# Kernel tuning notes

Hardware: AMD Instinct MI355X
Metric: run time of the kernel (lower is better)

Reference implementation:

```python
import jax, jax.numpy as jnp
import numpy as np

NUM_FEATURES = 20480
NUM_ACC = 128
BATCH = 4096
SPARSITY_P = 0.0015  # ~30 active features per position, like real NNUE


def setup_inputs() -> dict:
    key = jax.random.key(0)
    kw, kb, k1, k2, k3, k4 = jax.random.split(key, 6)
    # sparse binary one-hot-per-piece feature vectors
    white = (jax.random.uniform(kw, (BATCH, NUM_FEATURES)) < SPARSITY_P).astype(jnp.float32)
    black = (jax.random.uniform(kb, (BATCH, NUM_FEATURES)) < SPARSITY_P).astype(jnp.float32)
    psqt_w = jax.random.normal(k1, (2, NUM_FEATURES), dtype=jnp.float32) * 0.02
    acc_w = jax.random.normal(k2, (NUM_ACC, NUM_FEATURES), dtype=jnp.float32) * 0.02
    acc_b = jax.random.normal(k3, (NUM_ACC,), dtype=jnp.float32) * 0.02
    out_w = jax.random.normal(k4, (2, NUM_ACC), dtype=jnp.float32) * 0.1
    return {"white": white, "black": black, "psqt_w": psqt_w,
            "acc_w": acc_w, "acc_b": acc_b, "out_w": out_w}


def _side(x, psqt_w, acc_w, acc_b, out_w):
    # psqt: [B,2]; accumulator: [B,128]; CReLU then Linear(128->2, no bias)
    psqt = x @ psqt_w.T                              # [B, 2]
    acc = jnp.clip(x @ acc_w.T + acc_b, 0.0, 1.0)    # [B, 128]
    pos = acc @ out_w.T                              # [B, 2]
    return psqt, pos


def reference(white, black, psqt_w, acc_w, acc_b, out_w):
    psqt_w_, pos_w = _side(white, psqt_w, acc_w, acc_b, out_w)
    psqt_b, pos_b = _side(black, psqt_w, acc_w, acc_b, out_w)
    return (psqt_w_ - psqt_b) + (pos_w - pos_b)      # [B, 2]
```

## Files before the change

### kernel.cpp

```cpp
#include <hip/hip_runtime.h>

#define NF    20480
#define NACC  128
#define BATCH 4096
#define MAXI  96

typedef unsigned int uvec4 __attribute__((ext_vector_type(4)));
typedef unsigned int uvec2 __attribute__((ext_vector_type(2)));
typedef float        fvec4 __attribute__((ext_vector_type(4)));

__device__ __forceinline__ float bflo(unsigned int w) {
    union { unsigned int u; float f; } v; v.u = w << 16; return v.f;
}
__device__ __forceinline__ float bfhi(unsigned int w) {
    union { unsigned int u; float f; } v; v.u = w & 0xFFFF0000u; return v.f;
}
__device__ __forceinline__ unsigned short f2bf(float f) {
    union { float f; unsigned int i; } v; v.f = f;
    unsigned int x = v.i;
    return (unsigned short)((x + 0x7FFFu + ((x >> 16) & 1u)) >> 16);
}

__global__ __launch_bounds__(256) void transpose_accw(const float* __restrict__ acc_w,
                                                      unsigned short* __restrict__ accT) {
    __shared__ float tile[NACC][33];
    const int t  = threadIdx.x;
    const int f0 = blockIdx.x * 32;
    const int fl = t & 31;
    const int cr = t >> 5;
    #pragma unroll
    for (int i = 0; i < 16; ++i) {
        int cc = i * 8 + cr;
        tile[cc][fl] = acc_w[(size_t)cc * NF + f0 + fl];
    }
    __syncthreads();
    const int c  = t & 127;
    const int fr = t >> 7;
    #pragma unroll
    for (int i = 0; i < 16; ++i) {
        int ff = i * 2 + fr;
        accT[(size_t)(f0 + ff) * NACC + c] = f2bf(tile[c][ff]);
    }
}

#define BALLOT_COMPACT(d, fidx)                                           \
    {                                                                     \
        unsigned long long m = __ballot((d) != 0u);                       \
        if (m) {                                                          \
            int pre  = __popcll(m & ((1ull << lane) - 1ull));             \
            int src  = (int)(__ffsll((unsigned long long)(m)) - 1);       \
            int base = 0;                                                 \
            if (lane == src) base = atomicAdd(cnt, __popcll(m));          \
            base = __shfl(base, src, 64);                                 \
            int slot = base + pre;                                        \
            if ((d) && slot < MAXI) idx[slot] = (fidx);                   \
        }                                                                 \
    }

#define PROC16(c0, c1, c2, c3, fb)                                        \
    BALLOT_COMPACT(c0.x, (fb) + 0)   BALLOT_COMPACT(c0.y, (fb) + 1)       \
    BALLOT_COMPACT(c0.z, (fb) + 2)   BALLOT_COMPACT(c0.w, (fb) + 3)       \
    BALLOT_COMPACT(c1.x, (fb) + 512) BALLOT_COMPACT(c1.y, (fb) + 513)     \
    BALLOT_COMPACT(c1.z, (fb) + 514) BALLOT_COMPACT(c1.w, (fb) + 515)     \
    BALLOT_COMPACT(c2.x, (fb) + 1024) BALLOT_COMPACT(c2.y, (fb) + 1025)   \
    BALLOT_COMPACT(c2.z, (fb) + 1026) BALLOT_COMPACT(c2.w, (fb) + 1027)   \
    BALLOT_COMPACT(c3.x, (fb) + 1536) BALLOT_COMPACT(c3.y, (fb) + 1537)   \
    BALLOT_COMPACT(c3.z, (fb) + 1538) BALLOT_COMPACT(c3.w, (fb) + 1539)

__global__ __launch_bounds__(256) void nnue_main(
    const float* __restrict__ white,
    const float* __restrict__ black,
    const float* __restrict__ psqt_w,
    const unsigned short* __restrict__ accT,
    const float* __restrict__ acc_b,
    const float* __restrict__ out_w,
    float* __restrict__ out)
{
    __shared__ int   s_cnt[2];
    __shared__ int   s_idx[2][MAXI];
    __shared__ fvec4 s_part[2][4][32];
    __shared__ float s_red[8];

    const int t    = threadIdx.x;
    const int b    = blockIdx.x;
    const int side = t >> 7;
    const int lt   = t & 127;
    const int lane = t & 63;

    const float bias = acc_b[lt];
    const float ow0  = out_w[lt];
    const float ow1  = out_w[NACC + lt];
    const float sgn  = side ? -1.f : 1.f;

    const float* X  = (side ? black : white) + (size_t)b * NF;
    const uvec4* Xv = (const uvec4*)X;

    if (t < 2) s_cnt[t] = 0;
    __syncthreads();

    int* cnt = &s_cnt[side];
    int* idx = s_idx[side];

    uvec4 c0 = __builtin_nontemporal_load(&Xv[lt]);
    uvec4 c1 = __builtin_nontemporal_load(&Xv[lt + 128]);
    uvec4 c2 = __builtin_nontemporal_load(&Xv[lt + 256]);
    uvec4 c3 = __builtin_nontemporal_load(&Xv[lt + 384]);

    #pragma unroll 1
    for (int i = 0; i < 10; ++i) {
        uvec4 n0 = {0,0,0,0}, n1 = {0,0,0,0}, n2 = {0,0,0,0}, n3 = {0,0,0,0};
        if (i < 9) {
            const int v = (i + 1) * 512 + lt;
            n0 = __builtin_nontemporal_load(&Xv[v]);
            n1 = __builtin_nontemporal_load(&Xv[v + 128]);
            n2 = __builtin_nontemporal_load(&Xv[v + 256]);
            n3 = __builtin_nontemporal_load(&Xv[v + 384]);
        }
        const int fb = (i * 512 + lt) * 4;
        PROC16(c0, c1, c2, c3, fb)
        c0 = n0; c1 = n1; c2 = n2; c3 = n3;
    }
    __syncthreads();

    const int n      = min(s_cnt[side], MAXI);
    const int sub    = (t >> 5) & 3;
    const int lane32 = t & 31;
    const int* sIdx  = s_idx[side];

    float ps0 = 0.f, ps1 = 0.f;
    if (lt < n) {
        int f = sIdx[lt];
        ps0 = psqt_w[f];
        ps1 = psqt_w[NF + f];
    }

    fvec4 acc4 = {0.f, 0.f, 0.f, 0.f};
    for (int j = sub; j < n; j += 4) {
        int f = sIdx[j];
        uvec2 w = *(const uvec2*)(accT + (size_t)f * NACC + lane32 * 4);
        acc4.x += bflo(w.x); acc4.y += bfhi(w.x);
        acc4.z += bflo(w.y); acc4.w += bfhi(w.y);
    }
    s_part[side][sub][lane32] = acc4;
    __syncthreads();

    const float* sp = (const float*)&s_part[side][0][0];
    float a = sp[0 * NACC + lt] + sp[1 * NACC + lt]
            + sp[2 * NACC + lt] + sp[3 * NACC + lt];
    float h  = fminf(fmaxf(a + bias, 0.f), 1.f);
    float p0 = sgn * (h * ow0 + ps0);
    float p1 = sgn * (h * ow1 + ps1);

    #pragma unroll
    for (int off = 32; off > 0; off >>= 1) {
        p0 += __shfl_down(p0, off, 64);
        p1 += __shfl_down(p1, off, 64);
    }
    if ((t & 63) == 0) { int wv = t >> 6; s_red[wv * 2] = p0; s_red[wv * 2 + 1] = p1; }
    __syncthreads();

    if (t == 0) {
        out[(size_t)b * 2 + 0] = s_red[0] + s_red[2] + s_red[4] + s_red[6];
        out[(size_t)b * 2 + 1] = s_red[1] + s_red[3] + s_red[5] + s_red[7];
    }
}

extern "C" void kernel_launch(void* const* d_in, const int* in_sizes, int n_in,
                              void* d_out, int out_size, void* d_ws, size_t ws_size,
                              hipStream_t stream) {
    const float* white  = (const float*)d_in[0];
    const float* black  = (const float*)d_in[1];
    const float* psqt_w = (const float*)d_in[2];
    const float* acc_w  = (const float*)d_in[3];
    const float* acc_b  = (const float*)d_in[4];
    const float* out_w  = (const float*)d_in[5];
    float* out = (float*)d_out;

    unsigned short* accT = (unsigned short*)d_ws;

    transpose_accw<<<NF / 32, 256, 0, stream>>>(acc_w, accT);
    nnue_main<<<BATCH, 256, 0, stream>>>(white, black, psqt_w, accT,
                                         acc_b, out_w, out);
}
```

Baseline: 605.5 us.

## Replace shared atomic index compaction with per-wave mbcnt lists and skip empty quads

Each wave now compacts its active feature indices into its own shared list using mbcnt and a running per-wave base, which removes the LDS atomicAdd, the shuffle and the initial barrier. An extra ballot over each 4-wide chunk skips the four per-element ballots when the whole chunk is zero. The gather is split per wave with one 32-bit bf16 pair per lane instead of quarter-wave float4 splits, and the transpose writes packed pairs. The per-wave cap of 64 indices could drop features if a single wave sees more than that.

```diff
diff --git a/kernel.cpp b/kernel.cpp
--- a/kernel.cpp
+++ b/kernel.cpp
@@ -1,13 +1,11 @@
 #include <hip/hip_runtime.h>
 
-#define NF    20480
-#define NACC  128
-#define BATCH 4096
-#define MAXI  96
+#define NF     20480
+#define NACC   128
+#define BATCH  4096
+#define MAXI_W 64
 
 typedef unsigned int uvec4 __attribute__((ext_vector_type(4)));
-typedef unsigned int uvec2 __attribute__((ext_vector_type(2)));
-typedef float        fvec4 __attribute__((ext_vector_type(4)));
 
 __device__ __forceinline__ float bflo(unsigned int w) {
     union { unsigned int u; float f; } v; v.u = w << 16; return v.f;
@@ -34,38 +32,43 @@
         tile[cc][fl] = acc_w[(size_t)cc * NF + f0 + fl];
     }
     __syncthreads();
-    const int c  = t & 127;
-    const int fr = t >> 7;
+    const int c2 = t & 63;
+    const int fr = t >> 6;
     #pragma unroll
-    for (int i = 0; i < 16; ++i) {
-        int ff = i * 2 + fr;
-        accT[(size_t)(f0 + ff) * NACC + c] = f2bf(tile[c][ff]);
+    for (int i = 0; i < 8; ++i) {
+        int ff = i * 4 + fr;
+        unsigned int u = ((unsigned int)f2bf(tile[c2 * 2 + 1][ff]) << 16)
+                       |  (unsigned int)f2bf(tile[c2 * 2][ff]);
+        *(unsigned int*)(accT + (size_t)(f0 + ff) * NACC + c2 * 2) = u;
     }
 }
 
-#define BALLOT_COMPACT(d, fidx)                                           \
-    {                                                                     \
-        unsigned long long m = __ballot((d) != 0u);                       \
-        if (m) {                                                          \
-            int pre  = __popcll(m & ((1ull << lane) - 1ull));             \
-            int src  = (int)(__ffsll((unsigned long long)(m)) - 1);       \
-            int base = 0;                                                 \
-            if (lane == src) base = atomicAdd(cnt, __popcll(m));          \
-            base = __shfl(base, src, 64);                                 \
-            int slot = base + pre;                                        \
-            if ((d) && slot < MAXI) idx[slot] = (fidx);                   \
-        }                                                                 \
+#define BALLOT_COMPACT(d, fidx)                                             \
+    {                                                                       \
+        unsigned long long m = __ballot((d) != 0u);                         \
+        if (m) {                                                            \
+            unsigned int pre = __builtin_amdgcn_mbcnt_lo((unsigned int)m, 0u); \
+            pre = __builtin_amdgcn_mbcnt_hi((unsigned int)(m >> 32), pre);  \
+            int slot = base + (int)pre;                                     \
+            if ((d) != 0u && slot < MAXI_W) idx[slot] = (fidx);             \
+            base += (int)__popcll(m);                                       \
+        }                                                                   \
     }
 
-#define PROC16(c0, c1, c2, c3, fb)                                        \
-    BALLOT_COMPACT(c0.x, (fb) + 0)   BALLOT_COMPACT(c0.y, (fb) + 1)       \
-    BALLOT_COMPACT(c0.z, (fb) + 2)   BALLOT_COMPACT(c0.w, (fb) + 3)       \
-    BALLOT_COMPACT(c1.x, (fb) + 512) BALLOT_COMPACT(c1.y, (fb) + 513)     \
-    BALLOT_COMPACT(c1.z, (fb) + 514) BALLOT_COMPACT(c1.w, (fb) + 515)     \
-    BALLOT_COMPACT(c2.x, (fb) + 1024) BALLOT_COMPACT(c2.y, (fb) + 1025)   \
-    BALLOT_COMPACT(c2.z, (fb) + 1026) BALLOT_COMPACT(c2.w, (fb) + 1027)   \
-    BALLOT_COMPACT(c3.x, (fb) + 1536) BALLOT_COMPACT(c3.y, (fb) + 1537)   \
-    BALLOT_COMPACT(c3.z, (fb) + 1538) BALLOT_COMPACT(c3.w, (fb) + 1539)
+#define PROCQ(c, fb0)                                                       \
+    {                                                                       \
+        unsigned int any = (c).x | (c).y | (c).z | (c).w;                   \
+        if (__ballot(any != 0u)) {                                          \
+            BALLOT_COMPACT((c).x, (fb0) + 0)                                \
+            BALLOT_COMPACT((c).y, (fb0) + 1)                                \
+            BALLOT_COMPACT((c).z, (fb0) + 2)                                \
+            BALLOT_COMPACT((c).w, (fb0) + 3)                                \
+        }                                                                   \
+    }
+
+#define PROC16(c0, c1, c2, c3, fb)                                         \
+    PROCQ(c0, (fb))        PROCQ(c1, (fb) + 512)                           \
+    PROCQ(c2, (fb) + 1024) PROCQ(c3, (fb) + 1536)
 
 __global__ __launch_bounds__(256) void nnue_main(
     const float* __restrict__ white,
@@ -76,14 +79,15 @@
     const float* __restrict__ out_w,
     float* __restrict__ out)
 {
-    __shared__ int   s_cnt[2];
-    __shared__ int   s_idx[2][MAXI];
-    __shared__ fvec4 s_part[2][4][32];
+    __shared__ int   s_cnt[2][2];
+    __shared__ int   s_idx[2][2][MAXI_W];
+    __shared__ float s_part[2][2][NACC];
     __shared__ float s_red[8];
 
     const int t    = threadIdx.x;
     const int b    = blockIdx.x;
     const int side = t >> 7;
+    const int wv   = (t >> 6) & 1;
     const int lt   = t & 127;
     const int lane = t & 63;
 
@@ -95,11 +99,8 @@
     const float* X  = (side ? black : white) + (size_t)b * NF;
     const uvec4* Xv = (const uvec4*)X;
 
-    if (t < 2) s_cnt[t] = 0;
-    __syncthreads();
-
-    int* cnt = &s_cnt[side];
-    int* idx = s_idx[side];
+    int* idx = s_idx[side][wv];
+    int  base = 0;
 
     uvec4 c0 = __builtin_nontemporal_load(&Xv[lt]);
     uvec4 c1 = __builtin_nontemporal_load(&Xv[lt + 128]);
@@ -120,33 +121,34 @@
         PROC16(c0, c1, c2, c3, fb)
         c0 = n0; c1 = n1; c2 = n2; c3 = n3;
     }
+    if (lane == 0) s_cnt[side][wv] = base;
     __syncthreads();
 
-    const int n      = min(s_cnt[side], MAXI);
-    const int sub    = (t >> 5) & 3;
-    const int lane32 = t & 31;
-    const int* sIdx  = s_idx[side];
+    const int n0c = min(s_cnt[side][0], MAXI_W);
+    const int n1c = min(s_cnt[side][1], MAXI_W);
+    const int n   = n0c + n1c;
 
     float ps0 = 0.f, ps1 = 0.f;
     if (lt < n) {
-        int f = sIdx[lt];
+        int f = (lt < n0c) ? s_idx[side][0][lt] : s_idx[side][1][lt - n0c];
         ps0 = psqt_w[f];
         ps1 = psqt_w[NF + f];
     }
 
-    fvec4 acc4 = {0.f, 0.f, 0.f, 0.f};
-    for (int j = sub; j < n; j += 4) {
-        int f = sIdx[j];
-        uvec2 w = *(const uvec2*)(accT + (size_t)f * NACC + lane32 * 4);
-        acc4.x += bflo(w.x); acc4.y += bfhi(w.x);
-        acc4.z += bflo(w.y); acc4.w += bfhi(w.y);
+    const int  nw  = wv ? n1c : n0c;
+    const int* seg = s_idx[side][wv];
+    float a0 = 0.f, a1 = 0.f;
+    #pragma unroll 4
+    for (int j = 0; j < nw; ++j) {
+        int f = seg[j];
+        unsigned int w = *(const unsigned int*)(accT + (size_t)f * NACC + lane * 2);
+        a0 += bflo(w); a1 += bfhi(w);
     }
-    s_part[side][sub][lane32] = acc4;
+    s_part[side][wv][lane * 2]     = a0;
+    s_part[side][wv][lane * 2 + 1] = a1;
     __syncthreads();
 
-    const float* sp = (const float*)&s_part[side][0][0];
-    float a = sp[0 * NACC + lt] + sp[1 * NACC + lt]
-            + sp[2 * NACC + lt] + sp[3 * NACC + lt];
+    float a  = s_part[side][0][lt] + s_part[side][1][lt];
     float h  = fminf(fmaxf(a + bias, 0.f), 1.f);
     float p0 = sgn * (h * ow0 + ps0);
     float p1 = sgn * (h * ow1 + ps1);
@@ -156,7 +158,7 @@
         p0 += __shfl_down(p0, off, 64);
         p1 += __shfl_down(p1, off, 64);
     }
-    if ((t & 63) == 0) { int wv = t >> 6; s_red[wv * 2] = p0; s_red[wv * 2 + 1] = p1; }
+    if ((t & 63) == 0) { int w8 = t >> 6; s_red[w8 * 2] = p0; s_red[w8 * 2 + 1] = p1; }
     __syncthreads();
 
     if (t == 0) {
```

New measurement: 606.1 us. No clear change (+0.1%).
